# Kernel optimization log

Measured on AMD Instinct MI355X. Metric: run time of the kernel, lower is better.

Reference implementation:

```python
import jax, jax.numpy as jnp
import numpy as np
import math

DIM = 1024
NUM_HEADS = 16
HEAD_DIM = DIM // NUM_HEADS
B, S = 2, 2048

def setup_inputs() -> dict:
    key = jax.random.key(0)
    ks = jax.random.split(key, 9)
    sc = 0.02
    return {
        "x": jax.random.normal(ks[0], (B, S, DIM), jnp.float32),
        "Wq": jax.random.normal(ks[1], (DIM, DIM), jnp.float32) * sc,
        "bq": jax.random.normal(ks[2], (DIM,), jnp.float32) * sc,
        "Wk": jax.random.normal(ks[3], (DIM, DIM), jnp.float32) * sc,
        "bk": jax.random.normal(ks[4], (DIM,), jnp.float32) * sc,
        "Wv": jax.random.normal(ks[5], (DIM, DIM), jnp.float32) * sc,
        "bv": jax.random.normal(ks[6], (DIM,), jnp.float32) * sc,
        "Wo": jax.random.normal(ks[7], (DIM, DIM), jnp.float32) * sc,
        "bo": jax.random.normal(ks[8], (DIM,), jnp.float32) * sc,
    }

def reference(x, Wq, bq, Wk, bk, Wv, bv, Wo, bo):
    b, s, d = x.shape
    h, hd = NUM_HEADS, HEAD_DIM
    # qkv projections: [B,S,D] -> [B,H,S,hd]
    def split_heads(t):
        return t.reshape(b, s, h, hd).transpose(0, 2, 1, 3)
    q = split_heads(x @ Wq + bq)
    k = split_heads(x @ Wk + bk)
    v = split_heads(x @ Wv + bv)
    # scores [B,H,S,S], scale, causal mask via where(-10000), softmax
    scores = jnp.einsum('bhqd,bhkd->bhqk', q, k) / math.sqrt(hd)
    causal = jnp.tril(jnp.ones((s, s), dtype=bool))  # [S,S]
    scores = jnp.where(causal[None, None], scores, jnp.asarray(-10000.0, scores.dtype))
    probs = jax.nn.softmax(scores, axis=-1)
    ctx = jnp.einsum('bhqk,bhkd->bhqd', probs, v)
    ctx = ctx.transpose(0, 2, 1, 3).reshape(b, s, d)
    return ctx @ Wo + bo
```

## Files before the change

### kernel.cpp

```cpp
#include <hip/hip_runtime.h>
#include <hip/hip_bf16.h>

#define DIM 1024
#define NUM_HEADS 16
#define HEAD_DIM 64
#define BATCH 2
#define SEQ 2048
#define M_ROWS (BATCH * SEQ)

typedef short bh8 __attribute__((ext_vector_type(8)));
typedef float f32x4 __attribute__((ext_vector_type(4)));

#define SCALE_Q 0.18033688011116016f

__device__ __forceinline__ ushort f2bf(float f) {
    union { float f; unsigned u; } v; v.f = f;
    unsigned u = v.u;
    unsigned r = (u + 0x7FFFu + ((u >> 16) & 1u)) >> 16;
    return (ushort)r;
}

__device__ __forceinline__ ushort2 pk_bf16(float a, float b) {
#if __has_builtin(__builtin_amdgcn_cvt_pk_bf16_f32)
    auto r = __builtin_amdgcn_cvt_pk_bf16_f32(a, b);
    ushort2 o; __builtin_memcpy(&o, &r, 4); return o;
#else
    ushort2 o; o.x = f2bf(a); o.y = f2bf(b); return o;
#endif
}

__device__ __forceinline__ void async_cp16(const ushort* g, ushort* l) {
    __builtin_amdgcn_global_load_lds(
        (const __attribute__((address_space(1))) void*)(uintptr_t)g,
        (__attribute__((address_space(3))) void*)(uint32_t)(uintptr_t)l,
        16, 0, 0);
}

__global__ __launch_bounds__(256) void prep_inputs(
    const float* __restrict__ W0, const float* __restrict__ W1,
    const float* __restrict__ W2, const float* __restrict__ W3,
    const float* __restrict__ x,
    ushort* __restrict__ T0, ushort* __restrict__ T1,
    ushort* __restrict__ T2, ushort* __restrict__ T3,
    ushort* __restrict__ xb)
{
    const int z = blockIdx.z;
    const int t = threadIdx.x;
    if (z == 4) {
        int base = (blockIdx.y * 32 + blockIdx.x) * 1024 + t;
        const float4* in4 = (const float4*)x;
        ushort4* out4 = (ushort4*)xb;
        #pragma unroll
        for (int i = 0; i < 4; ++i) {
            float4 v = in4[base + i * 256];
            ushort4 o;
            o.x = f2bf(v.x); o.y = f2bf(v.y); o.z = f2bf(v.z); o.w = f2bf(v.w);
            out4[base + i * 256] = o;
        }
        return;
    }
    __shared__ float tile[32][33];
    const float* W = (z == 0) ? W0 : (z == 1) ? W1 : (z == 2) ? W2 : W3;
    ushort* Wt = (z == 0) ? T0 : (z == 1) ? T1 : (z == 2) ? T2 : T3;
    const int tx = t & 31, ty = t >> 5;
    const int k0 = blockIdx.y * 32, n0 = blockIdx.x * 32;
    #pragma unroll
    for (int i = 0; i < 4; ++i)
        tile[ty + 8 * i][tx] = W[(size_t)(k0 + ty + 8 * i) * DIM + n0 + tx];
    __syncthreads();
    #pragma unroll
    for (int i = 0; i < 4; ++i)
        Wt[(size_t)(n0 + ty + 8 * i) * DIM + k0 + tx] = f2bf(tile[tx][ty + 8 * i]);
}

#define GTM 128
#define GTN 64
#define GBK 64

__device__ __forceinline__ void gemm_core(
    const ushort* __restrict__ A, const ushort* __restrict__ Bt,
    ushort* smem, int m0, int n0, int t, f32x4 acc[4][2])
{
    ushort* As = smem;
    ushort* Bs = smem + 8192;
    const int lane = t & 63, wave = t >> 6;
    const int col = lane & 15, quad = lane >> 4;
    const int wm = (wave & 1) * 64, wn = (wave >> 1) * 32;

    for (int k0 = 0; k0 < DIM; k0 += GBK) {
        __syncthreads();
        #pragma unroll
        for (int j = 0; j < 4; ++j) {
            int C = wave * 256 + j * 64 + lane;
            int row = C >> 3;
            int lch = (C & 7) ^ (row & 7);
            async_cp16(&A[(size_t)(m0 + row) * DIM + k0 + lch * 8],
                       &As[(wave * 256 + j * 64) * 8]);
        }
        #pragma unroll
        for (int j = 0; j < 2; ++j) {
            int C = wave * 128 + j * 64 + lane;
            int row = C >> 3;
            int lch = (C & 7) ^ (row & 7);
            async_cp16(&Bt[(size_t)(n0 + row) * DIM + k0 + lch * 8],
                       &Bs[(wave * 128 + j * 64) * 8]);
        }
        __syncthreads();
        #pragma unroll
        for (int kk = 0; kk < 2; ++kk) {
            bh8 af[4], bfr[2];
            #pragma unroll
            for (int mi = 0; mi < 4; ++mi) {
                int row = wm + mi * 16 + col;
                af[mi] = *(const bh8*)&As[row * 64 + (((kk * 4 + quad) ^ (row & 7)) * 8)];
            }
            #pragma unroll
            for (int ni = 0; ni < 2; ++ni) {
                int row = wn + ni * 16 + col;
                bfr[ni] = *(const bh8*)&Bs[row * 64 + (((kk * 4 + quad) ^ (row & 7)) * 8)];
            }
            #pragma unroll
            for (int mi = 0; mi < 4; ++mi)
                #pragma unroll
                for (int ni = 0; ni < 2; ++ni)
                    acc[mi][ni] = __builtin_amdgcn_mfma_f32_16x16x32_bf16(
                        af[mi], bfr[ni], acc[mi][ni], 0, 0, 0);
        }
    }
}

__global__ __launch_bounds__(256) void gemm_qkv(
    const ushort* __restrict__ A,
    const ushort* __restrict__ WqT, const ushort* __restrict__ WkT,
    const ushort* __restrict__ WvT,
    const float* __restrict__ bq, const float* __restrict__ bk,
    const float* __restrict__ bv,
    ushort* __restrict__ qo, ushort* __restrict__ ko_, ushort* __restrict__ vo)
{
    __shared__ ushort smem[12288];
    const int z = blockIdx.z;
    const ushort* Bt = (z == 0) ? WqT : (z == 1) ? WkT : WvT;
    const float* bias = (z == 0) ? bq : (z == 1) ? bk : bv;
    ushort* outp = (z == 0) ? qo : (z == 1) ? ko_ : vo;

    const int t = threadIdx.x;
    const int lane = t & 63, wave = t >> 6;
    const int col = lane & 15, quad = lane >> 4;
    const int m0 = blockIdx.y * GTM, n0 = blockIdx.x * GTN;
    const int wm = (wave & 1) * 64, wn = (wave >> 1) * 32;
    f32x4 acc[4][2] = {};

    gemm_core(A, Bt, smem, m0, n0, t, acc);

    const int b = m0 >> 11, s0 = m0 & (SEQ - 1);
    const int h = n0 >> 6;

    if (z < 2) {
        const float scl = (z == 0) ? SCALE_Q : 1.f;
        __syncthreads();
        ushort* LT = smem;
        #pragma unroll
        for (int mi = 0; mi < 4; ++mi)
            #pragma unroll
            for (int ni = 0; ni < 2; ++ni) {
                int dl = wn + ni * 16 + col;
                float bvv = bias[n0 + dl];
                #pragma unroll
                for (int r = 0; r < 4; ++r) {
                    int ml = wm + mi * 16 + quad * 4 + r;
                    LT[ml * 72 + dl] = f2bf((acc[mi][ni][r] + bvv) * scl);
                }
            }
        __syncthreads();
        ushort* Cp = outp + (((size_t)(b * NUM_HEADS + h) * SEQ + s0) << 6);
        #pragma unroll
        for (int i = 0; i < 4; ++i) {
            int c = i * 256 + t;
            int row = c >> 3, ko = (c & 7) * 8;
            *(uint4*)&Cp[row * 64 + ko] = *(const uint4*)&LT[row * 72 + ko];
        }
    } else {
        __syncthreads();
        ushort* LT = smem;
        #pragma unroll
        for (int mi = 0; mi < 4; ++mi)
            #pragma unroll
            for (int ni = 0; ni < 2; ++ni) {
                int nl = wn + ni * 16 + col;
                float bvv = bias[n0 + nl];
                #pragma unroll
                for (int r = 0; r < 4; ++r) {
                    int ml = wm + mi * 16 + quad * 4 + r;
                    LT[nl * 136 + ml] = f2bf(acc[mi][ni][r] + bvv);
                }
            }
        __syncthreads();
        ushort* Cp = outp + (((size_t)(b * NUM_HEADS + h) * HEAD_DIM) << 11);
        #pragma unroll
        for (int i = 0; i < 4; ++i) {
            int c = i * 256 + t;
            int row = c >> 4, mo = (c & 15) * 8;
            *(uint4*)&Cp[((size_t)row << 11) + s0 + mo] = *(const uint4*)&LT[row * 136 + mo];
        }
    }
}

__global__ __launch_bounds__(256) void gemm_out(
    const ushort* __restrict__ A, const ushort* __restrict__ Bt,
    const float* __restrict__ bias, float* __restrict__ C)
{
    __shared__ ushort smem[12288];
    const int t = threadIdx.x;
    const int lane = t & 63, wave = t >> 6;
    const int col = lane & 15, quad = lane >> 4;
    const int m0 = blockIdx.y * GTM, n0 = blockIdx.x * GTN;
    const int wm = (wave & 1) * 64, wn = (wave >> 1) * 32;
    f32x4 acc[4][2] = {};

    gemm_core(A, Bt, smem, m0, n0, t, acc);

    #pragma unroll
    for (int mi = 0; mi < 4; ++mi)
        #pragma unroll
        for (int ni = 0; ni < 2; ++ni) {
            int n = n0 + wn + ni * 16 + col;
            float bvv = bias[n];
            #pragma unroll
            for (int r = 0; r < 4; ++r) {
                int m = m0 + wm + mi * 16 + quad * 4 + r;
                C[(size_t)m * DIM + n] = acc[mi][ni][r] + bvv;
            }
        }
}

#define PST 40

__global__ __launch_bounds__(256, 2) void attn_mfma(
    const ushort* __restrict__ Qg, const ushort* __restrict__ Kg,
    const ushort* __restrict__ Vtg, ushort* __restrict__ ctx)
{
    __shared__ char smem[34304];
    float* OA   = (float*)smem;
    float* OB   = (float*)(smem + 16640);
    float* lbuf = (float*)(smem + 33280);

    const int t = threadIdx.x;
    const int lane = t & 63, wave = t >> 6;
    const int col = lane & 15, quad = lane >> 4;
    const int bh = blockIdx.x & 31;
    const int qt = 31 - (blockIdx.x >> 5);
    const int b = bh >> 4, h = bh & 15;
    const int q0 = qt * 64;
    const int kw0 = wave * 32;
    const ushort* Kp = Kg + ((size_t)bh << 17);
    const ushort* Vp = Vtg + ((size_t)bh << 17);
    ushort* Pw = (ushort*)smem + wave * 64 * PST;

    bh8 qf[4][2];
    #pragma unroll
    for (int qi = 0; qi < 4; ++qi) {
        const ushort* Qp = Qg + ((size_t)bh << 17)
                         + ((size_t)(q0 + qi * 16 + col) << 6) + quad * 8;
        qf[qi][0] = *(const bh8*)(Qp);
        qf[qi][1] = *(const bh8*)(Qp + 32);
    }

    f32x4 O[4][4] = {};
    float l[4] = {0.f, 0.f, 0.f, 0.f};
    const int nIter = (q0 + 191) >> 7;

    bh8 kf_n[2][2], vf_n[4];
    #pragma unroll
    for (int kt = 0; kt < 2; ++kt)
        #pragma unroll
        for (int kk = 0; kk < 2; ++kk)
            kf_n[kt][kk] = *(const bh8*)&Kp[((size_t)(kw0 + kt * 16 + col) << 6) + kk * 32 + quad * 8];
    #pragma unroll
    for (int dt = 0; dt < 4; ++dt)
        vf_n[dt] = *(const bh8*)&Vp[((size_t)(dt * 16 + col) << 11) + kw0 + quad * 8];

    #pragma unroll 1
    for (int it = 0; it < nIter; ++it) {
        const int kb = it << 7;
        bh8 kf[2][2], vf[4];
        #pragma unroll
        for (int kt = 0; kt < 2; ++kt) { kf[kt][0] = kf_n[kt][0]; kf[kt][1] = kf_n[kt][1]; }
        #pragma unroll
        for (int dt = 0; dt < 4; ++dt) vf[dt] = vf_n[dt];

        if (it + 1 < nIter) {
            const int kb2 = kb + 128;
            #pragma unroll
            for (int kt = 0; kt < 2; ++kt)
                #pragma unroll
                for (int kk = 0; kk < 2; ++kk)
                    kf_n[kt][kk] = *(const bh8*)&Kp[((size_t)(kb2 + kw0 + kt * 16 + col) << 6) + kk * 32 + quad * 8];
            #pragma unroll
            for (int dt = 0; dt < 4; ++dt)
                vf_n[dt] = *(const bh8*)&Vp[((size_t)(dt * 16 + col) << 11) + kb2 + kw0 + quad * 8];
        }

        if (kb + kw0 > q0 + 63) continue;

        f32x4 St[2][4] = {};
        #pragma unroll
        for (int kk = 0; kk < 2; ++kk)
            #pragma unroll
            for (int kt = 0; kt < 2; ++kt)
                #pragma unroll
                for (int qi = 0; qi < 4; ++qi)
                    St[kt][qi] = __builtin_amdgcn_mfma_f32_16x16x32_bf16(
                        kf[kt][kk], qf[qi][kk], St[kt][qi], 0, 0, 0);

        if (kb + kw0 + 31 > q0) {
            #pragma unroll
            for (int kt = 0; kt < 2; ++kt)
                #pragma unroll
                for (int qi = 0; qi < 4; ++qi) {
                    int q_abs = q0 + qi * 16 + col;
                    #pragma unroll
                    for (int r = 0; r < 4; ++r)
                        if (kb + kw0 + kt * 16 + quad * 4 + r > q_abs) St[kt][qi][r] = -1e30f;
                }
        }

        #pragma unroll
        for (int kt = 0; kt < 2; ++kt)
            #pragma unroll
            for (int qi = 0; qi < 4; ++qi) {
                float p0 = exp2f(St[kt][qi][0]);
                float p1 = exp2f(St[kt][qi][1]);
                float p2 = exp2f(St[kt][qi][2]);
                float p3 = exp2f(St[kt][qi][3]);
                l[qi] += (p0 + p1) + (p2 + p3);
                ushort2 a01 = pk_bf16(p0, p1), a23 = pk_bf16(p2, p3);
                ushort4 pk4; pk4.x = a01.x; pk4.y = a01.y; pk4.z = a23.x; pk4.w = a23.y;
                *(ushort4*)&Pw[(qi * 16 + col) * PST + kt * 16 + quad * 4] = pk4;
            }

        bh8 pf[4];
        #pragma unroll
        for (int qi = 0; qi < 4; ++qi)
            pf[qi] = *(const bh8*)&Pw[(qi * 16 + col) * PST + quad * 8];
        #pragma unroll
        for (int dt = 0; dt < 4; ++dt)
            #pragma unroll
            for (int qi = 0; qi < 4; ++qi)
                O[dt][qi] = __builtin_amdgcn_mfma_f32_16x16x32_bf16(
                    vf[dt], pf[qi], O[dt][qi], 0, 0, 0);
    }

    #pragma unroll
    for (int qi = 0; qi < 4; ++qi) {
        l[qi] += __shfl_xor(l[qi], 16);
        l[qi] += __shfl_xor(l[qi], 32);
    }
    if (quad == 0) {
        #pragma unroll
        for (int qi = 0; qi < 4; ++qi)
            lbuf[wave * 64 + qi * 16 + col] = l[qi];
    }
    __syncthreads();

    if (wave == 1 || wave == 3) {
        float* dst = (wave == 1) ? OA : OB;
        #pragma unroll
        for (int dt = 0; dt < 4; ++dt)
            #pragma unroll
            for (int qi = 0; qi < 4; ++qi)
                #pragma unroll
                for (int r = 0; r < 4; ++r)
                    dst[(dt * 16 + quad * 4 + r) * 65 + qi * 16 + col] = O[dt][qi][r];
    }
    __syncthreads();
    if (wave == 0 || wave == 2) {
        float* src = (wave == 0) ? OA : OB;
        #pragma unroll
        for (int dt = 0; dt < 4; ++dt)
            #pragma unroll
            for (int qi = 0; qi < 4; ++qi)
                #pragma unroll
                for (int r = 0; r < 4; ++r)
                    O[dt][qi][r] += src[(dt * 16 + quad * 4 + r) * 65 + qi * 16 + col];
    }
    __syncthreads();
    if (wave == 2) {
        #pragma unroll
        for (int dt = 0; dt < 4; ++dt)
            #pragma unroll
            for (int qi = 0; qi < 4; ++qi)
                #pragma unroll
                for (int r = 0; r < 4; ++r)
                    OA[(dt * 16 + quad * 4 + r) * 65 + qi * 16 + col] = O[dt][qi][r];
    }
    __syncthreads();
    if (wave == 0) {
        float inv[4];
        #pragma unroll
        for (int qi = 0; qi < 4; ++qi) {
            int idx = qi * 16 + col;
            float lt = lbuf[idx] + lbuf[64 + idx] + lbuf[128 + idx] + lbuf[192 + idx];
            inv[qi] = 1.f / lt;
        }
        ushort* Oq = (ushort*)(smem + 16640);
        #pragma unroll
        for (int dt = 0; dt < 4; ++dt)
            #pragma unroll
            for (int qi = 0; qi < 4; ++qi) {
                float s0 = (O[dt][qi][0] + OA[(dt * 16 + quad * 4 + 0) * 65 + qi * 16 + col]) * inv[qi];
                float s1 = (O[dt][qi][1] + OA[(dt * 16 + quad * 4 + 1) * 65 + qi * 16 + col]) * inv[qi];
                float s2 = (O[dt][qi][2] + OA[(dt * 16 + quad * 4 + 2) * 65 + qi * 16 + col]) * inv[qi];
                float s3 = (O[dt][qi][3] + OA[(dt * 16 + quad * 4 + 3) * 65 + qi * 16 + col]) * inv[qi];
                ushort2 a01 = pk_bf16(s0, s1), a23 = pk_bf16(s2, s3);
                ushort4 pk4; pk4.x = a01.x; pk4.y = a01.y; pk4.z = a23.x; pk4.w = a23.y;
                *(ushort4*)&Oq[(qi * 16 + col) * 72 + dt * 16 + quad * 4] = pk4;
            }
        #pragma unroll
        for (int i = 0; i < 8; ++i) {
            int c = i * 64 + lane;
            int row = c >> 3, ko = (c & 7) * 8;
            *(uint4*)&ctx[((size_t)(b * SEQ) + q0 + row) * DIM + (h << 6) + ko] =
                *(const uint4*)&Oq[row * 72 + ko];
        }
    }
}

extern "C" void kernel_launch(void* const* d_in, const int* in_sizes, int n_in,
                              void* d_out, int out_size, void* d_ws, size_t ws_size,
                              hipStream_t stream) {
    const float* x  = (const float*)d_in[0];
    const float* Wq = (const float*)d_in[1];
    const float* bq = (const float*)d_in[2];
    const float* Wk = (const float*)d_in[3];
    const float* bk = (const float*)d_in[4];
    const float* Wv = (const float*)d_in[5];
    const float* bv = (const float*)d_in[6];
    const float* Wo = (const float*)d_in[7];
    const float* bo = (const float*)d_in[8];
    float* out = (float*)d_out;

    ushort* x_bf   = (ushort*)d_ws;
    ushort* wq_t   = x_bf + 4194304;
    ushort* wk_t   = wq_t + 1048576;
    ushort* wv_t   = wk_t + 1048576;
    ushort* wo_t   = wv_t + 1048576;
    ushort* q_ws   = wo_t + 1048576;
    ushort* k_ws   = q_ws + 4194304;
    ushort* vt_ws  = k_ws + 4194304;
    ushort* ctx_ws = vt_ws + 4194304;

    dim3 pgrid(32, 32, 5);
    prep_inputs<<<pgrid, 256, 0, stream>>>(Wq, Wk, Wv, Wo, x,
                                           wq_t, wk_t, wv_t, wo_t, x_bf);

    dim3 qkv_grid(DIM / GTN, M_ROWS / GTM, 3);
    gemm_qkv<<<qkv_grid, 256, 0, stream>>>(x_bf, wq_t, wk_t, wv_t,
                                           bq, bk, bv, q_ws, k_ws, vt_ws);

    attn_mfma<<<BATCH * NUM_HEADS * 32, 256, 0, stream>>>(q_ws, k_ws, vt_ws, ctx_ws);

    dim3 ogrid(DIM / GTN, M_ROWS / GTM);
    gemm_out<<<ogrid, 256, 0, stream>>>(ctx_ws, wo_t, bo, out);
}
```

Baseline: 192.8 us.

## Use 32x32 MFMA in attention with paired causal tiles and register P, widen QKV tiles

The attention kernel switches to 32x32x16 bf16 MFMA. Probabilities stay in registers and are rearranged with permlane32 swaps instead of an LDS round-trip, and each block now handles two query tiles (long and short causal) so work is balanced across a 512-block grid. The QKV projection GEMM grows its tile to 128x128 to get more operand reuse per block, at the cost of more LDS and registers. The changes trade extra register pressure and a serialized two-phase block for fewer LDS transfers and better load balance.

Result: slower. 201.7 us (+4.6%).

```diff
diff --git a/kernel.cpp b/kernel.cpp
--- a/kernel.cpp
+++ b/kernel.cpp
@@ -10,8 +10,18 @@
 
 typedef short bh8 __attribute__((ext_vector_type(8)));
 typedef float f32x4 __attribute__((ext_vector_type(4)));
+typedef float f32x16 __attribute__((ext_vector_type(16)));
 
 #define SCALE_Q 0.18033688011116016f
+
+#define MFMA16(a, b, c) __builtin_amdgcn_mfma_f32_16x16x32_bf16(a, b, c, 0, 0, 0)
+#define MFMA32(a, b, c) __builtin_amdgcn_mfma_f32_32x32x16_bf16(a, b, c, 0, 0, 0)
+
+#if __has_builtin(__builtin_amdgcn_exp2f)
+#define EXP2F(x) __builtin_amdgcn_exp2f(x)
+#else
+#define EXP2F(x) exp2f(x)
+#endif
 
 __device__ __forceinline__ ushort f2bf(float f) {
     union { float f; unsigned u; } v; v.f = f;
@@ -20,12 +30,24 @@
     return (ushort)r;
 }
 
-__device__ __forceinline__ ushort2 pk_bf16(float a, float b) {
-#if __has_builtin(__builtin_amdgcn_cvt_pk_bf16_f32)
-    auto r = __builtin_amdgcn_cvt_pk_bf16_f32(a, b);
-    ushort2 o; __builtin_memcpy(&o, &r, 4); return o;
+__device__ __forceinline__ unsigned cvt_pk_bf16(float lo, float hi) {
+    unsigned r;
+    asm("v_cvt_pk_bf16_f32 %0, %1, %2" : "=v"(r) : "v"(lo), "v"(hi));
+    return r;
+}
+
+__device__ __forceinline__ void plane_swap(unsigned a, unsigned b,
+                                           unsigned& o0, unsigned& o1, int h) {
+#if __has_builtin(__builtin_amdgcn_permlane32_swap)
+    (void)h;
+    auto pr = __builtin_amdgcn_permlane32_swap(a, b, false, false);
+    unsigned o[2]; __builtin_memcpy(o, &pr, 8);
+    o0 = o[0]; o1 = o[1];
 #else
-    ushort2 o; o.x = f2bf(a); o.y = f2bf(b); return o;
+    unsigned sa = (unsigned)__shfl_xor((int)a, 32);
+    unsigned sb = (unsigned)__shfl_xor((int)b, 32);
+    o0 = h ? sb : a;
+    o1 = h ? b : sa;
 #endif
 }
 
@@ -73,11 +95,58 @@
         Wt[(size_t)(n0 + ty + 8 * i) * DIM + k0 + tx] = f2bf(tile[tx][ty + 8 * i]);
 }
 
-#define GTM 128
-#define GTN 64
-#define GBK 64
-
-__device__ __forceinline__ void gemm_core(
+__device__ __forceinline__ void gemm_core128(
+    const ushort* __restrict__ A, const ushort* __restrict__ Bt,
+    ushort* smem, int m0, int n0, int t, f32x4 acc[4][4])
+{
+    ushort* As = smem;
+    ushort* Bs = smem + 8192;
+    const int lane = t & 63, wave = t >> 6;
+    const int col = lane & 15, quad = lane >> 4;
+    const int wm = (wave & 1) * 64, wn = (wave >> 1) * 64;
+
+    for (int k0 = 0; k0 < DIM; k0 += 64) {
+        __syncthreads();
+        #pragma unroll
+        for (int j = 0; j < 4; ++j) {
+            int C = wave * 256 + j * 64 + lane;
+            int row = C >> 3;
+            int lch = (C & 7) ^ (row & 7);
+            async_cp16(&A[(size_t)(m0 + row) * DIM + k0 + lch * 8],
+                       &As[(wave * 256 + j * 64) * 8]);
+        }
+        #pragma unroll
+        for (int j = 0; j < 4; ++j) {
+            int C = wave * 256 + j * 64 + lane;
+            int row = C >> 3;
+            int lch = (C & 7) ^ (row & 7);
+            async_cp16(&Bt[(size_t)(n0 + row) * DIM + k0 + lch * 8],
+                       &Bs[(wave * 256 + j * 64) * 8]);
+        }
+        __syncthreads();
+        #pragma unroll
+        for (int kk = 0; kk < 2; ++kk) {
+            bh8 af[4], bfr[4];
+            #pragma unroll
+            for (int mi = 0; mi < 4; ++mi) {
+                int row = wm + mi * 16 + col;
+                af[mi] = *(const bh8*)&As[row * 64 + (((kk * 4 + quad) ^ (row & 7)) * 8)];
+            }
+            #pragma unroll
+            for (int ni = 0; ni < 4; ++ni) {
+                int row = wn + ni * 16 + col;
+                bfr[ni] = *(const bh8*)&Bs[row * 64 + (((kk * 4 + quad) ^ (row & 7)) * 8)];
+            }
+            #pragma unroll
+            for (int mi = 0; mi < 4; ++mi)
+                #pragma unroll
+                for (int ni = 0; ni < 4; ++ni)
+                    acc[mi][ni] = MFMA16(af[mi], bfr[ni], acc[mi][ni]);
+        }
+    }
+}
+
+__device__ __forceinline__ void gemm_core64(
     const ushort* __restrict__ A, const ushort* __restrict__ Bt,
     ushort* smem, int m0, int n0, int t, f32x4 acc[4][2])
 {
@@ -87,7 +156,7 @@
     const int col = lane & 15, quad = lane >> 4;
     const int wm = (wave & 1) * 64, wn = (wave >> 1) * 32;
 
-    for (int k0 = 0; k0 < DIM; k0 += GBK) {
+    for (int k0 = 0; k0 < DIM; k0 += 64) {
         __syncthreads();
         #pragma unroll
         for (int j = 0; j < 4; ++j) {
@@ -123,8 +192,7 @@
             for (int mi = 0; mi < 4; ++mi)
                 #pragma unroll
                 for (int ni = 0; ni < 2; ++ni)
-                    acc[mi][ni] = __builtin_amdgcn_mfma_f32_16x16x32_bf16(
-                        af[mi], bfr[ni], acc[mi][ni], 0, 0, 0);
+                    acc[mi][ni] = MFMA16(af[mi], bfr[ni], acc[mi][ni]);
         }
     }
 }
@@ -137,7 +205,7 @@
     const float* __restrict__ bv,
     ushort* __restrict__ qo, ushort* __restrict__ ko_, ushort* __restrict__ vo)
 {
-    __shared__ ushort smem[12288];
+    __shared__ ushort smem[17408];
     const int z = blockIdx.z;
     const ushort* Bt = (z == 0) ? WqT : (z == 1) ? WkT : WvT;
     const float* bias = (z == 0) ? bq : (z == 1) ? bk : bv;
@@ -146,14 +214,13 @@
     const int t = threadIdx.x;
     const int lane = t & 63, wave = t >> 6;
     const int col = lane & 15, quad = lane >> 4;
-    const int m0 = blockIdx.y * GTM, n0 = blockIdx.x * GTN;
-    const int wm = (wave & 1) * 64, wn = (wave >> 1) * 32;
-    f32x4 acc[4][2] = {};
-
-    gemm_core(A, Bt, smem, m0, n0, t, acc);
+    const int m0 = blockIdx.y * 128, n0 = blockIdx.x * 128;
+    const int wm = (wave & 1) * 64, wn = (wave >> 1) * 64;
+    f32x4 acc[4][4] = {};
+
+    gemm_core128(A, Bt, smem, m0, n0, t, acc);
 
     const int b = m0 >> 11, s0 = m0 & (SEQ - 1);
-    const int h = n0 >> 6;
 
     if (z < 2) {
         const float scl = (z == 0) ? SCALE_Q : 1.f;
@@ -162,22 +229,23 @@
         #pragma unroll
         for (int mi = 0; mi < 4; ++mi)
             #pragma unroll
-            for (int ni = 0; ni < 2; ++ni) {
+            for (int ni = 0; ni < 4; ++ni) {
                 int dl = wn + ni * 16 + col;
                 float bvv = bias[n0 + dl];
                 #pragma unroll
                 for (int r = 0; r < 4; ++r) {
                     int ml = wm + mi * 16 + quad * 4 + r;
-                    LT[ml * 72 + dl] = f2bf((acc[mi][ni][r] + bvv) * scl);
+                    LT[ml * 136 + dl] = f2bf((acc[mi][ni][r] + bvv) * scl);
                 }
             }
         __syncthreads();
-        ushort* Cp = outp + (((size_t)(b * NUM_HEADS + h) * SEQ + s0) << 6);
-        #pragma unroll
-        for (int i = 0; i < 4; ++i) {
+        #pragma unroll
+        for (int i = 0; i < 8; ++i) {
             int c = i * 256 + t;
-            int row = c >> 3, ko = (c & 7) * 8;
-            *(uint4*)&Cp[row * 64 + ko] = *(const uint4*)&LT[row * 72 + ko];
+            int row = c >> 4, cg = (c & 15) * 8;
+            int hh = (n0 + cg) >> 6, d = (n0 + cg) & 63;
+            *(uint4*)&outp[((size_t)(b * NUM_HEADS + hh) * SEQ + s0 + row) * HEAD_DIM + d] =
+                *(const uint4*)&LT[row * 136 + cg];
         }
     } else {
         __syncthreads();
@@ -185,7 +253,7 @@
         #pragma unroll
         for (int mi = 0; mi < 4; ++mi)
             #pragma unroll
-            for (int ni = 0; ni < 2; ++ni) {
+            for (int ni = 0; ni < 4; ++ni) {
                 int nl = wn + ni * 16 + col;
                 float bvv = bias[n0 + nl];
                 #pragma unroll
@@ -195,12 +263,13 @@
                 }
             }
         __syncthreads();
-        ushort* Cp = outp + (((size_t)(b * NUM_HEADS + h) * HEAD_DIM) << 11);
-        #pragma unroll
-        for (int i = 0; i < 4; ++i) {
+        #pragma unroll
+        for (int i = 0; i < 8; ++i) {
             int c = i * 256 + t;
-            int row = c >> 4, mo = (c & 15) * 8;
-            *(uint4*)&Cp[((size_t)row << 11) + s0 + mo] = *(const uint4*)&LT[row * 136 + mo];
+            int drow = c >> 4, mo = (c & 15) * 8;
+            int hh = (n0 + drow) >> 6, d = (n0 + drow) & 63;
+            *(uint4*)&outp[(((size_t)(b * NUM_HEADS + hh) * HEAD_DIM + d) << 11) + s0 + mo] =
+                *(const uint4*)&LT[drow * 136 + mo];
         }
     }
 }
@@ -213,11 +282,11 @@
     const int t = threadIdx.x;
     const int lane = t & 63, wave = t >> 6;
     const int col = lane & 15, quad = lane >> 4;
-    const int m0 = blockIdx.y * GTM, n0 = blockIdx.x * GTN;
+    const int m0 = blockIdx.y * 128, n0 = blockIdx.x * 64;
     const int wm = (wave & 1) * 64, wn = (wave >> 1) * 32;
     f32x4 acc[4][2] = {};
 
-    gemm_core(A, Bt, smem, m0, n0, t, acc);
+    gemm_core64(A, Bt, smem, m0, n0, t, acc);
 
     #pragma unroll
     for (int mi = 0; mi < 4; ++mi)
@@ -232,8 +301,6 @@
             }
         }
 }
-
-#define PST 40
 
 __global__ __launch_bounds__(256, 2) void attn_mfma(
     const ushort* __restrict__ Qg, const ushort* __restrict__ Kg,
@@ -246,182 +313,196 @@
 
     const int t = threadIdx.x;
     const int lane = t & 63, wave = t >> 6;
-    const int col = lane & 15, quad = lane >> 4;
+    const int q32 = lane & 31, h = lane >> 5;
     const int bh = blockIdx.x & 31;
-    const int qt = 31 - (blockIdx.x >> 5);
-    const int b = bh >> 4, h = bh & 15;
-    const int q0 = qt * 64;
+    const int pi = blockIdx.x >> 5;
+    const int b = bh >> 4, hd = bh & 15;
     const int kw0 = wave * 32;
     const ushort* Kp = Kg + ((size_t)bh << 17);
     const ushort* Vp = Vtg + ((size_t)bh << 17);
-    ushort* Pw = (ushort*)smem + wave * 64 * PST;
-
-    bh8 qf[4][2];
-    #pragma unroll
-    for (int qi = 0; qi < 4; ++qi) {
-        const ushort* Qp = Qg + ((size_t)bh << 17)
-                         + ((size_t)(q0 + qi * 16 + col) << 6) + quad * 8;
-        qf[qi][0] = *(const bh8*)(Qp);
-        qf[qi][1] = *(const bh8*)(Qp + 32);
-    }
-
-    f32x4 O[4][4] = {};
-    float l[4] = {0.f, 0.f, 0.f, 0.f};
-    const int nIter = (q0 + 191) >> 7;
-
-    bh8 kf_n[2][2], vf_n[4];
-    #pragma unroll
-    for (int kt = 0; kt < 2; ++kt)
-        #pragma unroll
-        for (int kk = 0; kk < 2; ++kk)
-            kf_n[kt][kk] = *(const bh8*)&Kp[((size_t)(kw0 + kt * 16 + col) << 6) + kk * 32 + quad * 8];
-    #pragma unroll
-    for (int dt = 0; dt < 4; ++dt)
-        vf_n[dt] = *(const bh8*)&Vp[((size_t)(dt * 16 + col) << 11) + kw0 + quad * 8];
+    const ushort* Qp0 = Qg + ((size_t)bh << 17);
 
     #pragma unroll 1
-    for (int it = 0; it < nIter; ++it) {
-        const int kb = it << 7;
-        bh8 kf[2][2], vf[4];
-        #pragma unroll
-        for (int kt = 0; kt < 2; ++kt) { kf[kt][0] = kf_n[kt][0]; kf[kt][1] = kf_n[kt][1]; }
-        #pragma unroll
-        for (int dt = 0; dt < 4; ++dt) vf[dt] = vf_n[dt];
-
-        if (it + 1 < nIter) {
-            const int kb2 = kb + 128;
-            #pragma unroll
-            for (int kt = 0; kt < 2; ++kt)
-                #pragma unroll
-                for (int kk = 0; kk < 2; ++kk)
-                    kf_n[kt][kk] = *(const bh8*)&Kp[((size_t)(kb2 + kw0 + kt * 16 + col) << 6) + kk * 32 + quad * 8];
-            #pragma unroll
-            for (int dt = 0; dt < 4; ++dt)
-                vf_n[dt] = *(const bh8*)&Vp[((size_t)(dt * 16 + col) << 11) + kb2 + kw0 + quad * 8];
-        }
-
-        if (kb + kw0 > q0 + 63) continue;
-
-        f32x4 St[2][4] = {};
-        #pragma unroll
-        for (int kk = 0; kk < 2; ++kk)
-            #pragma unroll
-            for (int kt = 0; kt < 2; ++kt)
-                #pragma unroll
-                for (int qi = 0; qi < 4; ++qi)
-                    St[kt][qi] = __builtin_amdgcn_mfma_f32_16x16x32_bf16(
-                        kf[kt][kk], qf[qi][kk], St[kt][qi], 0, 0, 0);
-
-        if (kb + kw0 + 31 > q0) {
-            #pragma unroll
-            for (int kt = 0; kt < 2; ++kt)
-                #pragma unroll
-                for (int qi = 0; qi < 4; ++qi) {
-                    int q_abs = q0 + qi * 16 + col;
+    for (int ph = 0; ph < 2; ++ph) {
+        const int qt = ph ? pi : (31 - pi);
+        const int q0 = qt << 6;
+
+        bh8 qf[2][4];
+        #pragma unroll
+        for (int qti = 0; qti < 2; ++qti)
+            #pragma unroll
+            for (int kc = 0; kc < 4; ++kc)
+                qf[qti][kc] = *(const bh8*)&Qp0[((size_t)(q0 + qti * 32 + q32) << 6)
+                                                + kc * 16 + h * 8];
+
+        f32x16 O[2][2] = {};
+        float l[2] = {0.f, 0.f};
+        const int nIter = (q0 + 191) >> 7;
+
+        bh8 kf_n[4], vf_n[2][2];
+        #pragma unroll
+        for (int kc = 0; kc < 4; ++kc)
+            kf_n[kc] = *(const bh8*)&Kp[((size_t)(kw0 + q32) << 6) + kc * 16 + h * 8];
+        #pragma unroll
+        for (int dti = 0; dti < 2; ++dti)
+            #pragma unroll
+            for (int kc = 0; kc < 2; ++kc)
+                vf_n[dti][kc] = *(const bh8*)&Vp[((size_t)(dti * 32 + q32) << 11)
+                                                 + kw0 + kc * 16 + h * 8];
+
+        #pragma unroll 1
+        for (int it = 0; it < nIter; ++it) {
+            const int kb = it << 7;
+            bh8 kf[4], vf[2][2];
+            #pragma unroll
+            for (int kc = 0; kc < 4; ++kc) kf[kc] = kf_n[kc];
+            #pragma unroll
+            for (int dti = 0; dti < 2; ++dti) {
+                vf[dti][0] = vf_n[dti][0]; vf[dti][1] = vf_n[dti][1];
+            }
+
+            if (it + 1 < nIter) {
+                const int kb2 = kb + 128;
+                #pragma unroll
+                for (int kc = 0; kc < 4; ++kc)
+                    kf_n[kc] = *(const bh8*)&Kp[((size_t)(kb2 + kw0 + q32) << 6)
+                                                + kc * 16 + h * 8];
+                #pragma unroll
+                for (int dti = 0; dti < 2; ++dti)
                     #pragma unroll
-                    for (int r = 0; r < 4; ++r)
-                        if (kb + kw0 + kt * 16 + quad * 4 + r > q_abs) St[kt][qi][r] = -1e30f;
+                    for (int kc = 0; kc < 2; ++kc)
+                        vf_n[dti][kc] = *(const bh8*)&Vp[((size_t)(dti * 32 + q32) << 11)
+                                                         + kb2 + kw0 + kc * 16 + h * 8];
+            }
+
+            if (kb + kw0 > q0 + 63) continue;
+
+            f32x16 St[2] = {};
+            #pragma unroll
+            for (int kc = 0; kc < 4; ++kc) {
+                St[0] = MFMA32(kf[kc], qf[0][kc], St[0]);
+                St[1] = MFMA32(kf[kc], qf[1][kc], St[1]);
+            }
+
+            if (kb + kw0 + 31 > q0) {
+                #pragma unroll
+                for (int qti = 0; qti < 2; ++qti) {
+                    int q_abs = q0 + qti * 32 + q32;
+                    #pragma unroll
+                    for (int r = 0; r < 16; ++r) {
+                        int key_abs = kb + kw0 + (r & 3) + ((r >> 2) << 3) + 4 * h;
+                        if (key_abs > q_abs) St[qti][r] = -1e30f;
+                    }
                 }
-        }
-
-        #pragma unroll
-        for (int kt = 0; kt < 2; ++kt)
-            #pragma unroll
-            for (int qi = 0; qi < 4; ++qi) {
-                float p0 = exp2f(St[kt][qi][0]);
-                float p1 = exp2f(St[kt][qi][1]);
-                float p2 = exp2f(St[kt][qi][2]);
-                float p3 = exp2f(St[kt][qi][3]);
-                l[qi] += (p0 + p1) + (p2 + p3);
-                ushort2 a01 = pk_bf16(p0, p1), a23 = pk_bf16(p2, p3);
-                ushort4 pk4; pk4.x = a01.x; pk4.y = a01.y; pk4.z = a23.x; pk4.w = a23.y;
-                *(ushort4*)&Pw[(qi * 16 + col) * PST + kt * 16 + quad * 4] = pk4;
-            }
-
-        bh8 pf[4];
-        #pragma unroll
-        for (int qi = 0; qi < 4; ++qi)
-            pf[qi] = *(const bh8*)&Pw[(qi * 16 + col) * PST + quad * 8];
-        #pragma unroll
-        for (int dt = 0; dt < 4; ++dt)
-            #pragma unroll
-            for (int qi = 0; qi < 4; ++qi)
-                O[dt][qi] = __builtin_amdgcn_mfma_f32_16x16x32_bf16(
-                    vf[dt], pf[qi], O[dt][qi], 0, 0, 0);
-    }
-
-    #pragma unroll
-    for (int qi = 0; qi < 4; ++qi) {
-        l[qi] += __shfl_xor(l[qi], 16);
-        l[qi] += __shfl_xor(l[qi], 32);
-    }
-    if (quad == 0) {
-        #pragma unroll
-        for (int qi = 0; qi < 4; ++qi)
-            lbuf[wave * 64 + qi * 16 + col] = l[qi];
-    }
-    __syncthreads();
-
-    if (wave == 1 || wave == 3) {
-        float* dst = (wave == 1) ? OA : OB;
-        #pragma unroll
-        for (int dt = 0; dt < 4; ++dt)
-            #pragma unroll
-            for (int qi = 0; qi < 4; ++qi)
-                #pragma unroll
-                for (int r = 0; r < 4; ++r)
-                    dst[(dt * 16 + quad * 4 + r) * 65 + qi * 16 + col] = O[dt][qi][r];
-    }
-    __syncthreads();
-    if (wave == 0 || wave == 2) {
-        float* src = (wave == 0) ? OA : OB;
-        #pragma unroll
-        for (int dt = 0; dt < 4; ++dt)
-            #pragma unroll
-            for (int qi = 0; qi < 4; ++qi)
-                #pragma unroll
-                for (int r = 0; r < 4; ++r)
-                    O[dt][qi][r] += src[(dt * 16 + quad * 4 + r) * 65 + qi * 16 + col];
-    }
-    __syncthreads();
-    if (wave == 2) {
-        #pragma unroll
-        for (int dt = 0; dt < 4; ++dt)
-            #pragma unroll
-            for (int qi = 0; qi < 4; ++qi)
-                #pragma unroll
-                for (int r = 0; r < 4; ++r)
-                    OA[(dt * 16 + quad * 4 + r) * 65 + qi * 16 + col] = O[dt][qi][r];
-    }
-    __syncthreads();
-    if (wave == 0) {
-        float inv[4];
-        #pragma unroll
-        for (int qi = 0; qi < 4; ++qi) {
-            int idx = qi * 16 + col;
-            float lt = lbuf[idx] + lbuf[64 + idx] + lbuf[128 + idx] + lbuf[192 + idx];
-            inv[qi] = 1.f / lt;
-        }
-        ushort* Oq = (ushort*)(smem + 16640);
-        #pragma unroll
-        for (int dt = 0; dt < 4; ++dt)
-            #pragma unroll
-            for (int qi = 0; qi < 4; ++qi) {
-                float s0 = (O[dt][qi][0] + OA[(dt * 16 + quad * 4 + 0) * 65 + qi * 16 + col]) * inv[qi];
-                float s1 = (O[dt][qi][1] + OA[(dt * 16 + quad * 4 + 1) * 65 + qi * 16 + col]) * inv[qi];
-                float s2 = (O[dt][qi][2] + OA[(dt * 16 + quad * 4 + 2) * 65 + qi * 16 + col]) * inv[qi];
-                float s3 = (O[dt][qi][3] + OA[(dt * 16 + quad * 4 + 3) * 65 + qi * 16 + col]) * inv[qi];
-                ushort2 a01 = pk_bf16(s0, s1), a23 = pk_bf16(s2, s3);
-                ushort4 pk4; pk4.x = a01.x; pk4.y = a01.y; pk4.z = a23.x; pk4.w = a23.y;
-                *(ushort4*)&Oq[(qi * 16 + col) * 72 + dt * 16 + quad * 4] = pk4;
-            }
-        #pragma unroll
-        for (int i = 0; i < 8; ++i) {
-            int c = i * 64 + lane;
-            int row = c >> 3, ko = (c & 7) * 8;
-            *(uint4*)&ctx[((size_t)(b * SEQ) + q0 + row) * DIM + (h << 6) + ko] =
-                *(const uint4*)&Oq[row * 72 + ko];
-        }
+            }
+
+            #pragma unroll
+            for (int qti = 0; qti < 2; ++qti) {
+                float p[16];
+                #pragma unroll
+                for (int r = 0; r < 16; ++r) p[r] = EXP2F(St[qti][r]);
+                float t0 = (p[0] + p[1]) + (p[2] + p[3]);
+                float t1 = (p[4] + p[5]) + (p[6] + p[7]);
+                float t2 = (p[8] + p[9]) + (p[10] + p[11]);
+                float t3 = (p[12] + p[13]) + (p[14] + p[15]);
+                l[qti] += (t0 + t1) + (t2 + t3);
+
+                unsigned w[8];
+                #pragma unroll
+                for (int m = 0; m < 8; ++m) w[m] = cvt_pk_bf16(p[2 * m], p[2 * m + 1]);
+                unsigned j0, j1, j2, j3, j4, j5, j6, j7;
+                plane_swap(w[0], w[2], j0, j2, h);
+                plane_swap(w[1], w[3], j1, j3, h);
+                plane_swap(w[4], w[6], j4, j6, h);
+                plane_swap(w[5], w[7], j5, j7, h);
+                union { unsigned u[4]; bh8 v; } pu0, pu1;
+                pu0.u[0] = j0; pu0.u[1] = j1; pu0.u[2] = j2; pu0.u[3] = j3;
+                pu1.u[0] = j4; pu1.u[1] = j5; pu1.u[2] = j6; pu1.u[3] = j7;
+
+                O[qti][0] = MFMA32(vf[0][0], pu0.v, O[qti][0]);
+                O[qti][1] = MFMA32(vf[1][0], pu0.v, O[qti][1]);
+                O[qti][0] = MFMA32(vf[0][1], pu1.v, O[qti][0]);
+                O[qti][1] = MFMA32(vf[1][1], pu1.v, O[qti][1]);
+            }
+        }
+
+        l[0] += __shfl_xor(l[0], 32);
+        l[1] += __shfl_xor(l[1], 32);
+        if (lane < 32) {
+            lbuf[wave * 64 + q32]      = l[0];
+            lbuf[wave * 64 + 32 + q32] = l[1];
+        }
+        __syncthreads();
+
+        if (wave == 1 || wave == 3) {
+            float* dst = (wave == 1) ? OA : OB;
+            #pragma unroll
+            for (int qti = 0; qti < 2; ++qti)
+                #pragma unroll
+                for (int dti = 0; dti < 2; ++dti)
+                    #pragma unroll
+                    for (int r = 0; r < 16; ++r) {
+                        int d_l = dti * 32 + (r & 3) + ((r >> 2) << 3) + 4 * h;
+                        dst[d_l * 65 + qti * 32 + q32] = O[qti][dti][r];
+                    }
+        }
+        __syncthreads();
+        if (wave == 0 || wave == 2) {
+            float* src = (wave == 0) ? OA : OB;
+            #pragma unroll
+            for (int qti = 0; qti < 2; ++qti)
+                #pragma unroll
+                for (int dti = 0; dti < 2; ++dti)
+                    #pragma unroll
+                    for (int r = 0; r < 16; ++r) {
+                        int d_l = dti * 32 + (r & 3) + ((r >> 2) << 3) + 4 * h;
+                        O[qti][dti][r] += src[d_l * 65 + qti * 32 + q32];
+                    }
+        }
+        __syncthreads();
+        if (wave == 2) {
+            #pragma unroll
+            for (int qti = 0; qti < 2; ++qti)
+                #pragma unroll
+                for (int dti = 0; dti < 2; ++dti)
+                    #pragma unroll
+                    for (int r = 0; r < 16; ++r) {
+                        int d_l = dti * 32 + (r & 3) + ((r >> 2) << 3) + 4 * h;
+                        OA[d_l * 65 + qti * 32 + q32] = O[qti][dti][r];
+                    }
+        }
+        __syncthreads();
+        if (wave == 0) {
+            float tot0 = lbuf[q32] + lbuf[64 + q32] + lbuf[128 + q32] + lbuf[192 + q32];
+            float tot1 = lbuf[32 + q32] + lbuf[96 + q32] + lbuf[160 + q32] + lbuf[224 + q32];
+            float inv0 = 1.f / tot0, inv1 = 1.f / tot1;
+            ushort* Oq = (ushort*)(smem + 16640);
+            #pragma unroll
+            for (int qti = 0; qti < 2; ++qti) {
+                float invq = qti ? inv1 : inv0;
+                int qrow = qti * 32 + q32;
+                #pragma unroll
+                for (int dti = 0; dti < 2; ++dti)
+                    #pragma unroll
+                    for (int rg = 0; rg < 4; ++rg) {
+                        int d0 = dti * 32 + rg * 8 + 4 * h;
+                        float s0 = (O[qti][dti][rg * 4 + 0] + OA[(d0 + 0) * 65 + qrow]) * invq;
+                        float s1 = (O[qti][dti][rg * 4 + 1] + OA[(d0 + 1) * 65 + qrow]) * invq;
+                        float s2 = (O[qti][dti][rg * 4 + 2] + OA[(d0 + 2) * 65 + qrow]) * invq;
+                        float s3 = (O[qti][dti][rg * 4 + 3] + OA[(d0 + 3) * 65 + qrow]) * invq;
+                        uint2 pk; pk.x = cvt_pk_bf16(s0, s1); pk.y = cvt_pk_bf16(s2, s3);
+                        *(uint2*)&Oq[qrow * 72 + d0] = pk;
+                    }
+            }
+            #pragma unroll
+            for (int i = 0; i < 8; ++i) {
+                int c = i * 64 + lane;
+                int row = c >> 3, ko = (c & 7) * 8;
+                *(uint4*)&ctx[((size_t)(b * SEQ) + q0 + row) * DIM + (hd << 6) + ko] =
+                    *(const uint4*)&Oq[row * 72 + ko];
+            }
+        }
+        __syncthreads();
     }
 }
 
@@ -453,12 +534,12 @@
     prep_inputs<<<pgrid, 256, 0, stream>>>(Wq, Wk, Wv, Wo, x,
                                            wq_t, wk_t, wv_t, wo_t, x_bf);
 
-    dim3 qkv_grid(DIM / GTN, M_ROWS / GTM, 3);
+    dim3 qkv_grid(DIM / 128, M_ROWS / 128, 3);
     gemm_qkv<<<qkv_grid, 256, 0, stream>>>(x_bf, wq_t, wk_t, wv_t,
                                            bq, bk, bv, q_ws, k_ws, vt_ws);
 
-    attn_mfma<<<BATCH * NUM_HEADS * 32, 256, 0, stream>>>(q_ws, k_ws, vt_ws, ctx_ws);
-
-    dim3 ogrid(DIM / GTN, M_ROWS / GTM);
+    attn_mfma<<<512, 256, 0, stream>>>(q_ws, k_ws, vt_ws, ctx_ws);
+
+    dim3 ogrid(DIM / 64, M_ROWS / 128);
     gemm_out<<<ogrid, 256, 0, stream>>>(ctx_ws, wo_t, bo, out);
 }
```
